# Performance work log

Hardware: AMD Instinct MI355X
Metric: run time of the kernel (lower is better)

The kernel has to match this reference:

```python
import jax, jax.numpy as jnp
import numpy as np

NDIM = 4096      # ndim constructor arg; also hidden_node
BATCH = 2048
HID_F = 5        # hidden_feature (hardcoded in source)
STRIDE = 5       # encode_stride (hardcoded in source)


def _build_edges(ndim):
    # Faithful reproduction of the encoder edge construction in __init__.
    edges = []
    for j in range(ndim):
        c = j % ndim
        for i in range(c - STRIDE, c + STRIDE):
            edges.append([i % ndim, j])
    e = np.asarray(edges, dtype=np.int32).T  # [2, E], row=src, col=dst
    return e[0], e[1]


def setup_inputs() -> dict:
    key = jax.random.key(0)
    k1, k2, k3, k4, k5 = jax.random.split(key, 5)
    src, dst = _build_edges(NDIM)
    return {
        "x": jax.random.normal(k1, (BATCH, NDIM), jnp.float32),
        # PyG GraphConv((1, HID_F), HID_F): lin_rel Linear(1->HID_F, bias=True),
        # lin_root Linear(HID_F->HID_F, bias=False)
        "W_rel": jax.random.normal(k2, (HID_F, 1), jnp.float32) * 0.5,
        "b_rel": jax.random.normal(k3, (HID_F,), jnp.float32) * 0.1,
        "W_root": jax.random.normal(k4, (HID_F, HID_F), jnp.float32) * 0.1,
        # final Linear(ndim*HID_F -> ndim, bias=False)
        "W_final": jax.random.normal(k5, (NDIM, NDIM * HID_F), jnp.float32) * 0.01,
        "edge_src": jnp.asarray(src),
        "edge_dst": jnp.asarray(dst),
    }


def reference(x, W_rel, b_rel, W_root, W_final, edge_src, edge_dst):
    B, N = x.shape
    # gather source node features along edges: [B, E]
    vals = x[:, edge_src]
    # scatter-add into target nodes (sum aggregation): [B, N]
    agg = jax.ops.segment_sum(vals.T, edge_dst, num_segments=N).T
    # lin_rel (1 -> HID_F) applied to aggregated scalar feature
    z = agg[..., None] * W_rel[:, 0] + b_rel  # [B, N, HID_F]
    # lin_root applied to dst features z0 (zeros in this model) -- kept for faithfulness
    z0 = jnp.zeros((B, N, HID_F), x.dtype)
    z = z + z0 @ W_root.T
    z = jax.nn.relu(z)
    # final projection
    y = z.reshape(B, N * HID_F) @ W_final.T  # [B, N]
    return y
```

## Files before the change

### kernel.cpp

```cpp
#include <hip/hip_runtime.h>
#include <hip/hip_bf16.h>
#include <stdint.h>
#include <stddef.h>

#define NDIM  4096
#define BATCH 2048
#define HIDF  5
#define KDIM  (NDIM * HIDF)

typedef __bf16 bf16_t;
typedef __bf16 bf16x8 __attribute__((ext_vector_type(8)));
typedef float  f32x4  __attribute__((ext_vector_type(4)));

__device__ __forceinline__ void async_load_16B(const void* g, void* l) {
    __builtin_amdgcn_global_load_lds(
        (const __attribute__((address_space(1))) void*)g,
        (__attribute__((address_space(3))) void*)l,
        16, 0, 0);
}

__global__ void build_z(const float* __restrict__ x,
                        const float* __restrict__ W_rel,
                        const float* __restrict__ b_rel,
                        bf16_t* __restrict__ z)
{
    int idx = blockIdx.x * blockDim.x + threadIdx.x;
    int b = idx >> 12;
    int n = idx & (NDIM - 1);
    const float* xr = x + (size_t)b * NDIM;
    float agg = 0.f;
#pragma unroll
    for (int d = -5; d < 5; ++d)
        agg += xr[(n + d) & (NDIM - 1)];
    bf16_t* zr = z + (size_t)b * KDIM + n * HIDF;
#pragma unroll
    for (int f = 0; f < HIDF; ++f) {
        float v = fmaf(agg, W_rel[f], b_rel[f]);
        v = v > 0.f ? v : 0.f;
        zr[f] = (bf16_t)v;
    }
}

__global__ void cvt_w(const float* __restrict__ W, bf16_t* __restrict__ Wb,
                      int total8)
{
    int i = blockIdx.x * blockDim.x + threadIdx.x;
    int stride = gridDim.x * blockDim.x;
    for (; i < total8; i += stride) {
        const float* s = W + (size_t)i * 8;
        f32x4 v0 = *(const f32x4*)(s);
        f32x4 v1 = *(const f32x4*)(s + 4);
        bf16x8 pk;
        pk[0] = (bf16_t)v0[0]; pk[1] = (bf16_t)v0[1];
        pk[2] = (bf16_t)v0[2]; pk[3] = (bf16_t)v0[3];
        pk[4] = (bf16_t)v1[0]; pk[5] = (bf16_t)v1[1];
        pk[6] = (bf16_t)v1[2]; pk[7] = (bf16_t)v1[3];
        *(bf16x8*)(Wb + (size_t)i * 8) = pk;
    }
}

#define NT 160

__global__ __launch_bounds__(512, 2) void gemm8p(
    const bf16_t* __restrict__ Z,
    const bf16_t* __restrict__ Wb,
    float* __restrict__ Y,
    float* __restrict__ P)
{
    __shared__ char smem[131072];

    const int tid  = threadIdx.x;
    const int lane = tid & 63;
    const int wid  = tid >> 6;
    const int wr   = wid >> 2;
    const int wc   = wid & 3;

    const int bid   = blockIdx.x;
    const int split = bid & 1;
    const int tile  = bid >> 1;
    const int tm    = tile & 7;
    const int tn    = tile >> 3;
    const int m0    = tm * 256;
    const int n0    = tn * 256;
    const int kbase = split * (NT * 64);

    const int sr  = lane >> 3;
    const int scb = (lane & 7) ^ sr;
    const bf16_t* gA = Z  + (size_t)(m0 + wid * 8 + sr) * KDIM + kbase + scb * 8;
    const bf16_t* gB = Wb + (size_t)(n0 + wid * 8 + sr) * KDIM + kbase + scb * 8;

    const int r15  = lane & 15;
    const int xk   = (lane >> 4) << 4;
    const int xs   = (lane & 7) << 4;
    const int col0 = xk ^ xs;
    const int dcol = 64 - 2 * (col0 & 64);

    float* const out = split ? P : Y;

    f32x4 acc[8][4];
#pragma unroll
    for (int i = 0; i < 8; ++i)
#pragma unroll
        for (int j = 0; j < 4; ++j)
            acc[i][j] = (f32x4)0.f;

#pragma unroll
    for (int li = 0; li < 4; ++li) {
        async_load_16B(gA + (size_t)li * 64 * KDIM, smem + li * 8192 + wid * 1024);
        async_load_16B(gB + (size_t)li * 64 * KDIM, smem + 32768 + li * 8192 + wid * 1024);
    }

    for (int g = 0; g < NT; ++g) {
        char* const cb = smem + ((g & 1) ? 65536 : 0);
        char* const nb = smem + ((g & 1) ? 0 : 65536);
        const char* const pA = cb + (wr * 128 + r15) * 128 + col0;
        const char* const pB = cb + 32768 + (wc * 64 + r15) * 128 + col0;
        const bf16_t* const nA = gA + (size_t)(g + 1) * 64;
        const bf16_t* const nB = gB + (size_t)(g + 1) * 64;

        bf16x8 a[4][2], b[4][2];

        if (g + 1 < NT) {
            async_load_16B(nA, nb + wid * 1024);
            async_load_16B(nB, nb + 32768 + wid * 1024);
            asm volatile("s_waitcnt vmcnt(2)" ::: "memory");
        } else {
            asm volatile("s_waitcnt vmcnt(0)" ::: "memory");
        }
        __builtin_amdgcn_s_barrier();

#pragma unroll
        for (int mi = 0; mi < 4; ++mi) {
            a[mi][0] = *(const bf16x8*)(pA + mi * 2048);
            a[mi][1] = *(const bf16x8*)(pA + mi * 2048 + dcol);
        }
#pragma unroll
        for (int ni = 0; ni < 2; ++ni) {
            b[ni][0] = *(const bf16x8*)(pB + ni * 2048);
            b[ni][1] = *(const bf16x8*)(pB + ni * 2048 + dcol);
        }
        __builtin_amdgcn_s_barrier();
        asm volatile("s_waitcnt lgkmcnt(0)" ::: "memory");
        __builtin_amdgcn_sched_barrier(0);
        __builtin_amdgcn_s_setprio(1);
#pragma unroll
        for (int mi = 0; mi < 4; ++mi)
#pragma unroll
            for (int ni = 0; ni < 2; ++ni)
#pragma unroll
                for (int s = 0; s < 2; ++s)
                    acc[mi][ni] = __builtin_amdgcn_mfma_f32_16x16x32_bf16(
                        a[mi][s], b[ni][s], acc[mi][ni], 0, 0, 0);
        __builtin_amdgcn_s_setprio(0);
        __builtin_amdgcn_s_barrier();

#pragma unroll
        for (int ni = 2; ni < 4; ++ni) {
            b[ni][0] = *(const bf16x8*)(pB + ni * 2048);
            b[ni][1] = *(const bf16x8*)(pB + ni * 2048 + dcol);
        }
        if (g + 1 < NT) {
            async_load_16B(nA + (size_t)64 * KDIM, nb + 8192 + wid * 1024);
            async_load_16B(nB + (size_t)64 * KDIM, nb + 32768 + 8192 + wid * 1024);
        }
        __builtin_amdgcn_s_barrier();
        asm volatile("s_waitcnt lgkmcnt(0)" ::: "memory");
        __builtin_amdgcn_sched_barrier(0);
        __builtin_amdgcn_s_setprio(1);
#pragma unroll
        for (int mi = 0; mi < 4; ++mi)
#pragma unroll
            for (int ni = 2; ni < 4; ++ni)
#pragma unroll
                for (int s = 0; s < 2; ++s)
                    acc[mi][ni] = __builtin_amdgcn_mfma_f32_16x16x32_bf16(
                        a[mi][s], b[ni][s], acc[mi][ni], 0, 0, 0);
        __builtin_amdgcn_s_setprio(0);
        __builtin_amdgcn_s_barrier();

#pragma unroll
        for (int mi = 0; mi < 4; ++mi) {
            a[mi][0] = *(const bf16x8*)(pA + (mi + 4) * 2048);
            a[mi][1] = *(const bf16x8*)(pA + (mi + 4) * 2048 + dcol);
        }
        if (g + 1 < NT) {
            async_load_16B(nA + (size_t)128 * KDIM, nb + 16384 + wid * 1024);
            async_load_16B(nB + (size_t)128 * KDIM, nb + 32768 + 16384 + wid * 1024);
        }
        __builtin_amdgcn_s_barrier();
        asm volatile("s_waitcnt lgkmcnt(0)" ::: "memory");
        __builtin_amdgcn_sched_barrier(0);
        __builtin_amdgcn_s_setprio(1);
#pragma unroll
        for (int mi = 0; mi < 4; ++mi)
#pragma unroll
            for (int ni = 0; ni < 2; ++ni)
#pragma unroll
                for (int s = 0; s < 2; ++s)
                    acc[mi + 4][ni] = __builtin_amdgcn_mfma_f32_16x16x32_bf16(
                        a[mi][s], b[ni][s], acc[mi + 4][ni], 0, 0, 0);
        __builtin_amdgcn_s_setprio(0);
        __builtin_amdgcn_s_barrier();

        if (g + 1 < NT) {
            async_load_16B(nA + (size_t)192 * KDIM, nb + 24576 + wid * 1024);
            async_load_16B(nB + (size_t)192 * KDIM, nb + 32768 + 24576 + wid * 1024);
        }
        __builtin_amdgcn_s_barrier();
        __builtin_amdgcn_s_setprio(1);
#pragma unroll
        for (int mi = 0; mi < 4; ++mi)
#pragma unroll
            for (int ni = 2; ni < 4; ++ni)
#pragma unroll
                for (int s = 0; s < 2; ++s)
                    acc[mi + 4][ni] = __builtin_amdgcn_mfma_f32_16x16x32_bf16(
                        a[mi][s], b[ni][s], acc[mi + 4][ni], 0, 0, 0);
        __builtin_amdgcn_s_setprio(0);
        __builtin_amdgcn_s_barrier();
    }

    const int crow = m0 + wr * 128 + (lane >> 4) * 4;
    const int ccol = n0 + wc * 64 + (lane & 15);
#pragma unroll
    for (int mi = 0; mi < 8; ++mi)
#pragma unroll
        for (int ni = 0; ni < 4; ++ni) {
            float* cp = out + (size_t)(crow + mi * 16) * NDIM + ccol + ni * 16;
#pragma unroll
            for (int rr = 0; rr < 4; ++rr)
                cp[(size_t)rr * NDIM] = acc[mi][ni][rr];
        }
}

__global__ void add_y(float* __restrict__ y, const float* __restrict__ p, int n4)
{
    int i = blockIdx.x * blockDim.x + threadIdx.x;
    int st = gridDim.x * blockDim.x;
    for (; i < n4; i += st) {
        f32x4 a = ((const f32x4*)y)[i];
        f32x4 b = ((const f32x4*)p)[i];
        ((f32x4*)y)[i] = a + b;
    }
}

#define BM 128
#define BN 128
#define BK 64

__global__ __launch_bounds__(256) void gemm_bb(
    const bf16_t* __restrict__ Z,
    const bf16_t* __restrict__ Wb,
    float*        __restrict__ Y)
{
    __shared__ bf16_t As[BM * BK];
    __shared__ bf16_t Bs[BN * BK];

    const int tid  = threadIdx.x;
    const int lane = tid & 63;
    const int wid  = tid >> 6;
    const int bidm = blockIdx.x & 15;
    const int bidn = blockIdx.x >> 4;
    const int bm0 = bidm * BM;
    const int bn0 = bidn * BN;
    const int wr = wid >> 1, wc = wid & 1;

    f32x4 acc[4][4];
#pragma unroll
    for (int i = 0; i < 4; ++i)
#pragma unroll
        for (int j = 0; j < 4; ++j)
            acc[i][j] = (f32x4)0.f;

    const int arow_l = lane >> 3;
    const int acol_l = (lane & 7) * 8;

    for (int kt = 0; kt < KDIM / BK; ++kt) {
        const int k0 = kt * BK;
#pragma unroll
        for (int r = 0; r < 4; ++r) {
            const int chunk = wid * 4 + r;
            const int row   = chunk * 8 + arow_l;
            async_load_16B(Z + (size_t)(bm0 + row) * KDIM + k0 + acol_l,
                           (void*)(As + chunk * 512));
            async_load_16B(Wb + (size_t)(bn0 + row) * KDIM + k0 + acol_l,
                           (void*)(Bs + chunk * 512));
        }
        __syncthreads();
#pragma unroll
        for (int s = 0; s < 2; ++s) {
            bf16x8 af[4], bfr[4];
            const int ko = s * 32 + (lane >> 4) * 8;
#pragma unroll
            for (int mi = 0; mi < 4; ++mi)
                af[mi] = *(const bf16x8*)(As + (wr * 64 + mi * 16 + (lane & 15)) * BK + ko);
#pragma unroll
            for (int ni = 0; ni < 4; ++ni)
                bfr[ni] = *(const bf16x8*)(Bs + (wc * 64 + ni * 16 + (lane & 15)) * BK + ko);
#pragma unroll
            for (int mi = 0; mi < 4; ++mi)
#pragma unroll
                for (int ni = 0; ni < 4; ++ni)
                    acc[mi][ni] = __builtin_amdgcn_mfma_f32_16x16x32_bf16(
                        af[mi], bfr[ni], acc[mi][ni], 0, 0, 0);
        }
        __syncthreads();
    }

    const int crow = bm0 + wr * 64 + (lane >> 4) * 4;
    const int ccol = bn0 + wc * 64 + (lane & 15);
#pragma unroll
    for (int mi = 0; mi < 4; ++mi)
#pragma unroll
        for (int ni = 0; ni < 4; ++ni) {
            float* cp = Y + (size_t)(crow + mi * 16) * NDIM + ccol + ni * 16;
#pragma unroll
            for (int r = 0; r < 4; ++r)
                cp[(size_t)r * NDIM] = acc[mi][ni][r];
        }
}

__global__ __launch_bounds__(256) void gemm_zw(
    const bf16_t* __restrict__ Z,
    const float*  __restrict__ W,
    float*        __restrict__ Y)
{
    __shared__ bf16_t As[BM * BK];
    __shared__ bf16_t Bs[BN * BK];

    const int tid  = threadIdx.x;
    const int lane = tid & 63;
    const int wid  = tid >> 6;
    const int bidm = blockIdx.x & 15;
    const int bidn = blockIdx.x >> 4;
    const int bm0 = bidm * BM;
    const int bn0 = bidn * BN;
    const int wr = wid >> 1, wc = wid & 1;

    f32x4 acc[4][4];
#pragma unroll
    for (int i = 0; i < 4; ++i)
#pragma unroll
        for (int j = 0; j < 4; ++j)
            acc[i][j] = (f32x4)0.f;

    const int arow_l = lane >> 3;
    const int acol_l = (lane & 7) * 8;

    for (int kt = 0; kt < KDIM / BK; ++kt) {
        const int k0 = kt * BK;
#pragma unroll
        for (int r = 0; r < 4; ++r) {
            const int chunk = wid * 4 + r;
            const int row   = chunk * 8 + arow_l;
            async_load_16B(Z + (size_t)(bm0 + row) * KDIM + k0 + acol_l,
                           (void*)(As + chunk * 512));
        }
#pragma unroll
        for (int r = 0; r < 4; ++r) {
            const int chunk = wid * 4 + r;
            const int row   = chunk * 8 + arow_l;
            const float* src = W + (size_t)(bn0 + row) * KDIM + k0 + acol_l;
            f32x4 v0 = *(const f32x4*)(src);
            f32x4 v1 = *(const f32x4*)(src + 4);
            bf16x8 pk;
            pk[0] = (bf16_t)v0[0]; pk[1] = (bf16_t)v0[1];
            pk[2] = (bf16_t)v0[2]; pk[3] = (bf16_t)v0[3];
            pk[4] = (bf16_t)v1[0]; pk[5] = (bf16_t)v1[1];
            pk[6] = (bf16_t)v1[2]; pk[7] = (bf16_t)v1[3];
            *(bf16x8*)(Bs + chunk * 512 + lane * 8) = pk;
        }
        __syncthreads();
#pragma unroll
        for (int s = 0; s < 2; ++s) {
            bf16x8 af[4], bfr[4];
            const int ko = s * 32 + (lane >> 4) * 8;
#pragma unroll
            for (int mi = 0; mi < 4; ++mi)
                af[mi] = *(const bf16x8*)(As + (wr * 64 + mi * 16 + (lane & 15)) * BK + ko);
#pragma unroll
            for (int ni = 0; ni < 4; ++ni)
                bfr[ni] = *(const bf16x8*)(Bs + (wc * 64 + ni * 16 + (lane & 15)) * BK + ko);
#pragma unroll
            for (int mi = 0; mi < 4; ++mi)
#pragma unroll
                for (int ni = 0; ni < 4; ++ni)
                    acc[mi][ni] = __builtin_amdgcn_mfma_f32_16x16x32_bf16(
                        af[mi], bfr[ni], acc[mi][ni], 0, 0, 0);
        }
        __syncthreads();
    }

    const int crow = bm0 + wr * 64 + (lane >> 4) * 4;
    const int ccol = bn0 + wc * 64 + (lane & 15);
#pragma unroll
    for (int mi = 0; mi < 4; ++mi)
#pragma unroll
        for (int ni = 0; ni < 4; ++ni) {
            float* cp = Y + (size_t)(crow + mi * 16) * NDIM + ccol + ni * 16;
#pragma unroll
            for (int r = 0; r < 4; ++r)
                cp[(size_t)r * NDIM] = acc[mi][ni][r];
        }
}

extern "C" void kernel_launch(void* const* d_in, const int* in_sizes, int n_in,
                              void* d_out, int out_size, void* d_ws, size_t ws_size,
                              hipStream_t stream)
{
    const float* x      = (const float*)d_in[0];
    const float* W_rel  = (const float*)d_in[1];
    const float* b_rel  = (const float*)d_in[2];
    const float* W_fin  = (const float*)d_in[4];

    const size_t z_bytes  = (size_t)BATCH * KDIM * sizeof(bf16_t);
    const size_t wb_bytes = (size_t)NDIM  * KDIM * sizeof(bf16_t);
    const size_t p_bytes  = (size_t)BATCH * NDIM * sizeof(float);

    char* ws = (char*)d_ws;
    bf16_t* z  = (bf16_t*)ws;
    float*  y  = (float*)d_out;

    build_z<<<(BATCH * NDIM) / 256, 256, 0, stream>>>(x, W_rel, b_rel, z);

    if (ws_size >= z_bytes + wb_bytes + p_bytes) {
        bf16_t* Wb = (bf16_t*)(ws + z_bytes);
        float*  P  = (float*)(ws + z_bytes + wb_bytes);
        cvt_w<<<2048, 256, 0, stream>>>(W_fin, Wb, (int)((size_t)NDIM * KDIM / 8));
        gemm8p<<<256, 512, 0, stream>>>(z, Wb, y, P);
        add_y<<<2048, 256, 0, stream>>>(y, P, (BATCH * NDIM) / 4);
    } else if (ws_size >= z_bytes + wb_bytes) {
        bf16_t* Wb = (bf16_t*)(ws + z_bytes);
        cvt_w<<<2048, 256, 0, stream>>>(W_fin, Wb, (int)((size_t)NDIM * KDIM / 8));
        gemm_bb<<<(NDIM / BN) * (BATCH / BM), 256, 0, stream>>>(z, Wb, y);
    } else {
        gemm_zw<<<(NDIM / BN) * (BATCH / BM), 256, 0, stream>>>(z, W_fin, y);
    }
}
```

Measured before the change: 447.8 us.

## Replace four-phase ping-pong GEMM loop with simple double-buffered K-loop

Replaces the interleaved four-phase schedule (split LDS reads, staged async prefetches, setprio and sched_barrier fences) with a plain double-buffered loop. Each iteration issues all eight next-tile async loads up front, waits on the current buffer, loads all A/B fragments from LDS, and runs the full 8x4 MFMA block before one barrier. This removes many barriers and priority toggles. In exchange it loses fine-grained overlap of LDS reads with MFMAs and needs more registers for fragments.

```diff
diff --git a/kernel.cpp b/kernel.cpp
--- a/kernel.cpp
+++ b/kernel.cpp
@@ -115,109 +115,42 @@
         char* const nb = smem + ((g & 1) ? 0 : 65536);
         const char* const pA = cb + (wr * 128 + r15) * 128 + col0;
         const char* const pB = cb + 32768 + (wc * 64 + r15) * 128 + col0;
-        const bf16_t* const nA = gA + (size_t)(g + 1) * 64;
-        const bf16_t* const nB = gB + (size_t)(g + 1) * 64;
-
-        bf16x8 a[4][2], b[4][2];
 
         if (g + 1 < NT) {
-            async_load_16B(nA, nb + wid * 1024);
-            async_load_16B(nB, nb + 32768 + wid * 1024);
-            asm volatile("s_waitcnt vmcnt(2)" ::: "memory");
+            const bf16_t* const nA = gA + (size_t)(g + 1) * 64;
+            const bf16_t* const nB = gB + (size_t)(g + 1) * 64;
+#pragma unroll
+            for (int li = 0; li < 4; ++li) {
+                async_load_16B(nA + (size_t)li * 64 * KDIM, nb + li * 8192 + wid * 1024);
+                async_load_16B(nB + (size_t)li * 64 * KDIM, nb + 32768 + li * 8192 + wid * 1024);
+            }
+            asm volatile("s_waitcnt vmcnt(8)" ::: "memory");
         } else {
             asm volatile("s_waitcnt vmcnt(0)" ::: "memory");
         }
-        __builtin_amdgcn_s_barrier();
-
-#pragma unroll
-        for (int mi = 0; mi < 4; ++mi) {
+        asm volatile("s_barrier" ::: "memory");
+
+        bf16x8 a[8][2], b[4][2];
+#pragma unroll
+        for (int ni = 0; ni < 4; ++ni) {
+            b[ni][0] = *(const bf16x8*)(pB + ni * 2048);
+            b[ni][1] = *(const bf16x8*)(pB + ni * 2048 + dcol);
+        }
+#pragma unroll
+        for (int mi = 0; mi < 8; ++mi) {
             a[mi][0] = *(const bf16x8*)(pA + mi * 2048);
             a[mi][1] = *(const bf16x8*)(pA + mi * 2048 + dcol);
         }
 #pragma unroll
-        for (int ni = 0; ni < 2; ++ni) {
-            b[ni][0] = *(const bf16x8*)(pB + ni * 2048);
-            b[ni][1] = *(const bf16x8*)(pB + ni * 2048 + dcol);
-        }
-        __builtin_amdgcn_s_barrier();
-        asm volatile("s_waitcnt lgkmcnt(0)" ::: "memory");
-        __builtin_amdgcn_sched_barrier(0);
-        __builtin_amdgcn_s_setprio(1);
-#pragma unroll
-        for (int mi = 0; mi < 4; ++mi)
-#pragma unroll
-            for (int ni = 0; ni < 2; ++ni)
+        for (int mi = 0; mi < 8; ++mi)
+#pragma unroll
+            for (int ni = 0; ni < 4; ++ni)
 #pragma unroll
                 for (int s = 0; s < 2; ++s)
                     acc[mi][ni] = __builtin_amdgcn_mfma_f32_16x16x32_bf16(
                         a[mi][s], b[ni][s], acc[mi][ni], 0, 0, 0);
-        __builtin_amdgcn_s_setprio(0);
-        __builtin_amdgcn_s_barrier();
-
-#pragma unroll
-        for (int ni = 2; ni < 4; ++ni) {
-            b[ni][0] = *(const bf16x8*)(pB + ni * 2048);
-            b[ni][1] = *(const bf16x8*)(pB + ni * 2048 + dcol);
-        }
-        if (g + 1 < NT) {
-            async_load_16B(nA + (size_t)64 * KDIM, nb + 8192 + wid * 1024);
-            async_load_16B(nB + (size_t)64 * KDIM, nb + 32768 + 8192 + wid * 1024);
-        }
-        __builtin_amdgcn_s_barrier();
-        asm volatile("s_waitcnt lgkmcnt(0)" ::: "memory");
-        __builtin_amdgcn_sched_barrier(0);
-        __builtin_amdgcn_s_setprio(1);
-#pragma unroll
-        for (int mi = 0; mi < 4; ++mi)
-#pragma unroll
-            for (int ni = 2; ni < 4; ++ni)
-#pragma unroll
-                for (int s = 0; s < 2; ++s)
-                    acc[mi][ni] = __builtin_amdgcn_mfma_f32_16x16x32_bf16(
-                        a[mi][s], b[ni][s], acc[mi][ni], 0, 0, 0);
-        __builtin_amdgcn_s_setprio(0);
-        __builtin_amdgcn_s_barrier();
-
-#pragma unroll
-        for (int mi = 0; mi < 4; ++mi) {
-            a[mi][0] = *(const bf16x8*)(pA + (mi + 4) * 2048);
-            a[mi][1] = *(const bf16x8*)(pA + (mi + 4) * 2048 + dcol);
-        }
-        if (g + 1 < NT) {
-            async_load_16B(nA + (size_t)128 * KDIM, nb + 16384 + wid * 1024);
-            async_load_16B(nB + (size_t)128 * KDIM, nb + 32768 + 16384 + wid * 1024);
-        }
-        __builtin_amdgcn_s_barrier();
-        asm volatile("s_waitcnt lgkmcnt(0)" ::: "memory");
-        __builtin_amdgcn_sched_barrier(0);
-        __builtin_amdgcn_s_setprio(1);
-#pragma unroll
-        for (int mi = 0; mi < 4; ++mi)
-#pragma unroll
-            for (int ni = 0; ni < 2; ++ni)
-#pragma unroll
-                for (int s = 0; s < 2; ++s)
-                    acc[mi + 4][ni] = __builtin_amdgcn_mfma_f32_16x16x32_bf16(
-                        a[mi][s], b[ni][s], acc[mi + 4][ni], 0, 0, 0);
-        __builtin_amdgcn_s_setprio(0);
-        __builtin_amdgcn_s_barrier();
-
-        if (g + 1 < NT) {
-            async_load_16B(nA + (size_t)192 * KDIM, nb + 24576 + wid * 1024);
-            async_load_16B(nB + (size_t)192 * KDIM, nb + 32768 + 24576 + wid * 1024);
-        }
-        __builtin_amdgcn_s_barrier();
-        __builtin_amdgcn_s_setprio(1);
-#pragma unroll
-        for (int mi = 0; mi < 4; ++mi)
-#pragma unroll
-            for (int ni = 2; ni < 4; ++ni)
-#pragma unroll
-                for (int s = 0; s < 2; ++s)
-                    acc[mi + 4][ni] = __builtin_amdgcn_mfma_f32_16x16x32_bf16(
-                        a[mi][s], b[ni][s], acc[mi + 4][ni], 0, 0, 0);
-        __builtin_amdgcn_s_setprio(0);
-        __builtin_amdgcn_s_barrier();
+
+        asm volatile("s_barrier" ::: "memory");
     }
 
     const int crow = m0 + wr * 128 + (lane >> 4) * 4;
```

New measurement: 453.2 us. Within noise of the previous version (+1.2%).

## Fuse fp32-to-bf16 weight conversion into the split-K GEMM B-tile load path

Applied to the files above, without the earlier changes.

Drops the separate cvt_w pass that turned W_final into a bf16 workspace copy. The GEMM now reads fp32 weights through registers, converts them to bf16 and writes the swizzled layout into LDS. It also restructures the prefetch so all A loads and B register loads are issued at the top of each iteration. This removes one full read-write pass over the 64M-element weight, but each weight tile is now read in fp32 by every M-tile block (8x per N-tile), and the loads are synchronous register loads that must wait on vmcnt(0) before the LDS store.

```diff
diff --git a/kernel.cpp b/kernel.cpp
--- a/kernel.cpp
+++ b/kernel.cpp
@@ -41,29 +41,11 @@
     }
 }
 
-__global__ void cvt_w(const float* __restrict__ W, bf16_t* __restrict__ Wb,
-                      int total8)
-{
-    int i = blockIdx.x * blockDim.x + threadIdx.x;
-    int stride = gridDim.x * blockDim.x;
-    for (; i < total8; i += stride) {
-        const float* s = W + (size_t)i * 8;
-        f32x4 v0 = *(const f32x4*)(s);
-        f32x4 v1 = *(const f32x4*)(s + 4);
-        bf16x8 pk;
-        pk[0] = (bf16_t)v0[0]; pk[1] = (bf16_t)v0[1];
-        pk[2] = (bf16_t)v0[2]; pk[3] = (bf16_t)v0[3];
-        pk[4] = (bf16_t)v1[0]; pk[5] = (bf16_t)v1[1];
-        pk[6] = (bf16_t)v1[2]; pk[7] = (bf16_t)v1[3];
-        *(bf16x8*)(Wb + (size_t)i * 8) = pk;
-    }
-}
-
 #define NT 160
 
-__global__ __launch_bounds__(512, 2) void gemm8p(
+__global__ __launch_bounds__(512, 2) void gemm_f(
     const bf16_t* __restrict__ Z,
-    const bf16_t* __restrict__ Wb,
+    const float*  __restrict__ W,
     float* __restrict__ Y,
     float* __restrict__ P)
 {
@@ -85,13 +67,15 @@
     const int kbase = split * (NT * 64);
 
     const int sr  = lane >> 3;
-    const int scb = (lane & 7) ^ sr;
-    const bf16_t* gA = Z  + (size_t)(m0 + wid * 8 + sr) * KDIM + kbase + scb * 8;
-    const bf16_t* gB = Wb + (size_t)(n0 + wid * 8 + sr) * KDIM + kbase + scb * 8;
+    const int l7  = lane & 7;
+    const int scb = l7 ^ sr;
+    const bf16_t* gA = Z + (size_t)(m0 + wid * 8 + sr) * KDIM + kbase + scb * 8;
+
+    const float* gBf = W + (size_t)(n0 + wid * 32 + sr) * KDIM + kbase + l7 * 8;
 
     const int r15  = lane & 15;
     const int xk   = (lane >> 4) << 4;
-    const int xs   = (lane & 7) << 4;
+    const int xs   = l7 << 4;
     const int col0 = xk ^ xs;
     const int dcol = 64 - 2 * (col0 & 64);
 
@@ -104,30 +88,48 @@
         for (int j = 0; j < 4; ++j)
             acc[i][j] = (f32x4)0.f;
 
+    f32x4 bv[4][2];
+
 #pragma unroll
     for (int li = 0; li < 4; ++li) {
         async_load_16B(gA + (size_t)li * 64 * KDIM, smem + li * 8192 + wid * 1024);
-        async_load_16B(gB + (size_t)li * 64 * KDIM, smem + 32768 + li * 8192 + wid * 1024);
-    }
+        const float* s = gBf + (size_t)li * 8 * KDIM;
+        bv[li][0] = *(const f32x4*)(s);
+        bv[li][1] = *(const f32x4*)(s + 4);
+    }
+    asm volatile("s_waitcnt vmcnt(0)" ::: "memory");
+#pragma unroll
+    for (int li = 0; li < 4; ++li) {
+        bf16x8 pk;
+#pragma unroll
+        for (int j = 0; j < 4; ++j) {
+            pk[j]     = (bf16_t)bv[li][0][j];
+            pk[j + 4] = (bf16_t)bv[li][1][j];
+        }
+        *(bf16x8*)(smem + 32768 + (wid * 4 + li) * 1024 + sr * 128 + scb * 16) = pk;
+    }
+    asm volatile("s_waitcnt lgkmcnt(0)" ::: "memory");
 
     for (int g = 0; g < NT; ++g) {
         char* const cb = smem + ((g & 1) ? 65536 : 0);
         char* const nb = smem + ((g & 1) ? 0 : 65536);
         const char* const pA = cb + (wr * 128 + r15) * 128 + col0;
         const char* const pB = cb + 32768 + (wc * 64 + r15) * 128 + col0;
-        const bf16_t* const nA = gA + (size_t)(g + 1) * 64;
-        const bf16_t* const nB = gB + (size_t)(g + 1) * 64;
 
         bf16x8 a[4][2], b[4][2];
 
         if (g + 1 < NT) {
-            async_load_16B(nA, nb + wid * 1024);
-            async_load_16B(nB, nb + 32768 + wid * 1024);
-            asm volatile("s_waitcnt vmcnt(2)" ::: "memory");
-        } else {
-            asm volatile("s_waitcnt vmcnt(0)" ::: "memory");
-        }
-        __builtin_amdgcn_s_barrier();
+            const bf16_t* const nA = gA + (size_t)(g + 1) * 64;
+            const float*  const nB = gBf + (size_t)(g + 1) * 64;
+#pragma unroll
+            for (int li = 0; li < 4; ++li) {
+                async_load_16B(nA + (size_t)li * 64 * KDIM, nb + li * 8192 + wid * 1024);
+                const float* s = nB + (size_t)li * 8 * KDIM;
+                bv[li][0] = *(const f32x4*)(s);
+                bv[li][1] = *(const f32x4*)(s + 4);
+            }
+        }
+        asm volatile("s_barrier" ::: "memory");
 
 #pragma unroll
         for (int mi = 0; mi < 4; ++mi) {
@@ -139,7 +141,7 @@
             b[ni][0] = *(const bf16x8*)(pB + ni * 2048);
             b[ni][1] = *(const bf16x8*)(pB + ni * 2048 + dcol);
         }
-        __builtin_amdgcn_s_barrier();
+        asm volatile("s_barrier" ::: "memory");
         asm volatile("s_waitcnt lgkmcnt(0)" ::: "memory");
         __builtin_amdgcn_sched_barrier(0);
         __builtin_amdgcn_s_setprio(1);
@@ -152,18 +154,14 @@
                     acc[mi][ni] = __builtin_amdgcn_mfma_f32_16x16x32_bf16(
                         a[mi][s], b[ni][s], acc[mi][ni], 0, 0, 0);
         __builtin_amdgcn_s_setprio(0);
-        __builtin_amdgcn_s_barrier();
+        asm volatile("s_barrier" ::: "memory");
 
 #pragma unroll
         for (int ni = 2; ni < 4; ++ni) {
             b[ni][0] = *(const bf16x8*)(pB + ni * 2048);
             b[ni][1] = *(const bf16x8*)(pB + ni * 2048 + dcol);
         }
-        if (g + 1 < NT) {
-            async_load_16B(nA + (size_t)64 * KDIM, nb + 8192 + wid * 1024);
-            async_load_16B(nB + (size_t)64 * KDIM, nb + 32768 + 8192 + wid * 1024);
-        }
-        __builtin_amdgcn_s_barrier();
+        asm volatile("s_barrier" ::: "memory");
         asm volatile("s_waitcnt lgkmcnt(0)" ::: "memory");
         __builtin_amdgcn_sched_barrier(0);
         __builtin_amdgcn_s_setprio(1);
@@ -176,7 +174,7 @@
                     acc[mi][ni] = __builtin_amdgcn_mfma_f32_16x16x32_bf16(
                         a[mi][s], b[ni][s], acc[mi][ni], 0, 0, 0);
         __builtin_amdgcn_s_setprio(0);
-        __builtin_amdgcn_s_barrier();
+        asm volatile("s_barrier" ::: "memory");
 
 #pragma unroll
         for (int mi = 0; mi < 4; ++mi) {
@@ -184,10 +182,19 @@
             a[mi][1] = *(const bf16x8*)(pA + (mi + 4) * 2048 + dcol);
         }
         if (g + 1 < NT) {
-            async_load_16B(nA + (size_t)128 * KDIM, nb + 16384 + wid * 1024);
-            async_load_16B(nB + (size_t)128 * KDIM, nb + 32768 + 16384 + wid * 1024);
-        }
-        __builtin_amdgcn_s_barrier();
+            asm volatile("s_waitcnt vmcnt(0)" ::: "memory");
+#pragma unroll
+            for (int li = 0; li < 4; ++li) {
+                bf16x8 pk;
+#pragma unroll
+                for (int j = 0; j < 4; ++j) {
+                    pk[j]     = (bf16_t)bv[li][0][j];
+                    pk[j + 4] = (bf16_t)bv[li][1][j];
+                }
+                *(bf16x8*)(nb + 32768 + (wid * 4 + li) * 1024 + sr * 128 + scb * 16) = pk;
+            }
+        }
+        asm volatile("s_barrier" ::: "memory");
         asm volatile("s_waitcnt lgkmcnt(0)" ::: "memory");
         __builtin_amdgcn_sched_barrier(0);
         __builtin_amdgcn_s_setprio(1);
@@ -200,13 +207,9 @@
                     acc[mi + 4][ni] = __builtin_amdgcn_mfma_f32_16x16x32_bf16(
                         a[mi][s], b[ni][s], acc[mi + 4][ni], 0, 0, 0);
         __builtin_amdgcn_s_setprio(0);
-        __builtin_amdgcn_s_barrier();
-
-        if (g + 1 < NT) {
-            async_load_16B(nA + (size_t)192 * KDIM, nb + 24576 + wid * 1024);
-            async_load_16B(nB + (size_t)192 * KDIM, nb + 32768 + 24576 + wid * 1024);
-        }
-        __builtin_amdgcn_s_barrier();
+        asm volatile("s_barrier" ::: "memory");
+
+        asm volatile("s_barrier" ::: "memory");
         __builtin_amdgcn_s_setprio(1);
 #pragma unroll
         for (int mi = 0; mi < 4; ++mi)
@@ -217,7 +220,7 @@
                     acc[mi + 4][ni] = __builtin_amdgcn_mfma_f32_16x16x32_bf16(
                         a[mi][s], b[ni][s], acc[mi + 4][ni], 0, 0, 0);
         __builtin_amdgcn_s_setprio(0);
-        __builtin_amdgcn_s_barrier();
+        asm volatile("s_barrier" ::: "memory");
     }
 
     const int crow = m0 + wr * 128 + (lane >> 4) * 4;
@@ -247,78 +250,6 @@
 #define BM 128
 #define BN 128
 #define BK 64
-
-__global__ __launch_bounds__(256) void gemm_bb(
-    const bf16_t* __restrict__ Z,
-    const bf16_t* __restrict__ Wb,
-    float*        __restrict__ Y)
-{
-    __shared__ bf16_t As[BM * BK];
-    __shared__ bf16_t Bs[BN * BK];
-
-    const int tid  = threadIdx.x;
-    const int lane = tid & 63;
-    const int wid  = tid >> 6;
-    const int bidm = blockIdx.x & 15;
-    const int bidn = blockIdx.x >> 4;
-    const int bm0 = bidm * BM;
-    const int bn0 = bidn * BN;
-    const int wr = wid >> 1, wc = wid & 1;
-
-    f32x4 acc[4][4];
-#pragma unroll
-    for (int i = 0; i < 4; ++i)
-#pragma unroll
-        for (int j = 0; j < 4; ++j)
-            acc[i][j] = (f32x4)0.f;
-
-    const int arow_l = lane >> 3;
-    const int acol_l = (lane & 7) * 8;
-
-    for (int kt = 0; kt < KDIM / BK; ++kt) {
-        const int k0 = kt * BK;
-#pragma unroll
-        for (int r = 0; r < 4; ++r) {
-            const int chunk = wid * 4 + r;
-            const int row   = chunk * 8 + arow_l;
-            async_load_16B(Z + (size_t)(bm0 + row) * KDIM + k0 + acol_l,
-                           (void*)(As + chunk * 512));
-            async_load_16B(Wb + (size_t)(bn0 + row) * KDIM + k0 + acol_l,
-                           (void*)(Bs + chunk * 512));
-        }
-        __syncthreads();
-#pragma unroll
-        for (int s = 0; s < 2; ++s) {
-            bf16x8 af[4], bfr[4];
-            const int ko = s * 32 + (lane >> 4) * 8;
-#pragma unroll
-            for (int mi = 0; mi < 4; ++mi)
-                af[mi] = *(const bf16x8*)(As + (wr * 64 + mi * 16 + (lane & 15)) * BK + ko);
-#pragma unroll
-            for (int ni = 0; ni < 4; ++ni)
-                bfr[ni] = *(const bf16x8*)(Bs + (wc * 64 + ni * 16 + (lane & 15)) * BK + ko);
-#pragma unroll
-            for (int mi = 0; mi < 4; ++mi)
-#pragma unroll
-                for (int ni = 0; ni < 4; ++ni)
-                    acc[mi][ni] = __builtin_amdgcn_mfma_f32_16x16x32_bf16(
-                        af[mi], bfr[ni], acc[mi][ni], 0, 0, 0);
-        }
-        __syncthreads();
-    }
-
-    const int crow = bm0 + wr * 64 + (lane >> 4) * 4;
-    const int ccol = bn0 + wc * 64 + (lane & 15);
-#pragma unroll
-    for (int mi = 0; mi < 4; ++mi)
-#pragma unroll
-        for (int ni = 0; ni < 4; ++ni) {
-            float* cp = Y + (size_t)(crow + mi * 16) * NDIM + ccol + ni * 16;
-#pragma unroll
-            for (int r = 0; r < 4; ++r)
-                cp[(size_t)r * NDIM] = acc[mi][ni][r];
-        }
-}
 
 __global__ __launch_bounds__(256) void gemm_zw(
     const bf16_t* __restrict__ Z,
@@ -413,9 +344,8 @@
     const float* b_rel  = (const float*)d_in[2];
     const float* W_fin  = (const float*)d_in[4];
 
-    const size_t z_bytes  = (size_t)BATCH * KDIM * sizeof(bf16_t);
-    const size_t wb_bytes = (size_t)NDIM  * KDIM * sizeof(bf16_t);
-    const size_t p_bytes  = (size_t)BATCH * NDIM * sizeof(float);
+    const size_t z_bytes = (size_t)BATCH * KDIM * sizeof(bf16_t);
+    const size_t p_bytes = (size_t)BATCH * NDIM * sizeof(float);
 
     char* ws = (char*)d_ws;
     bf16_t* z  = (bf16_t*)ws;
@@ -423,16 +353,10 @@
 
     build_z<<<(BATCH * NDIM) / 256, 256, 0, stream>>>(x, W_rel, b_rel, z);
 
-    if (ws_size >= z_bytes + wb_bytes + p_bytes) {
-        bf16_t* Wb = (bf16_t*)(ws + z_bytes);
-        float*  P  = (float*)(ws + z_bytes + wb_bytes);
-        cvt_w<<<2048, 256, 0, stream>>>(W_fin, Wb, (int)((size_t)NDIM * KDIM / 8));
-        gemm8p<<<256, 512, 0, stream>>>(z, Wb, y, P);
+    if (ws_size >= z_bytes + p_bytes) {
+        float* P = (float*)(ws + z_bytes);
+        gemm_f<<<256, 512, 0, stream>>>(z, W_fin, y, P);
         add_y<<<2048, 256, 0, stream>>>(y, P, (BATCH * NDIM) / 4);
-    } else if (ws_size >= z_bytes + wb_bytes) {
-        bf16_t* Wb = (bf16_t*)(ws + z_bytes);
-        cvt_w<<<2048, 256, 0, stream>>>(W_fin, Wb, (int)((size_t)NDIM * KDIM / 8));
-        gemm_bb<<<(NDIM / BN) * (BATCH / BM), 256, 0, stream>>>(z, Wb, y);
     } else {
         gemm_zw<<<(NDIM / BN) * (BATCH / BM), 256, 0, stream>>>(z, W_fin, y);
     }
```

After: 509.8 us. +13.8%, slower.
